# Kernel tuning notes

Hardware: AMD Instinct MI355X
Metric: run time of the kernel (lower is better)

Reference implementation:

```python
import jax, jax.numpy as jnp
import numpy as np

EPS = 1e-14  # clamp floor from torch .clamp(1e-14)


def setup_inputs() -> dict:
    key = jax.random.key(0)
    kq, kk, kv, km = jax.random.split(key, 4)
    B, L, D = 16, 2048, 64
    q = jax.random.normal(kq, (B, L, D), dtype=jnp.float32)
    k = jax.random.normal(kk, (B, L, D), dtype=jnp.float32)
    v = jax.random.normal(kv, (B, L, D), dtype=jnp.float32)
    # boolean mask, True = masked-out position (score forced to 0 in 'dot' mode)
    attn_mask = jax.random.randint(km, (B, L, L), 0, 2).astype(jnp.bool_)
    return {"q": q, "k": k, "v": v, "attn_mask": attn_mask}


def reference(q, k, v, attn_mask):
    # kernel_type='dot': raw QK^T scores (no temperature scaling)
    attn = jnp.einsum('bqd,bkd->bqk', q, k)
    # masked positions set to 0 (not -inf) in the 'dot' path
    attn = jnp.where(attn_mask, jnp.zeros((), attn.dtype), attn)
    # sum-normalization instead of softmax: attn / attn.sum(-1).clamp(1e-14)
    denom = jnp.clip(jnp.sum(attn, axis=2, keepdims=True), EPS)
    attn = attn / denom
    # dropout is identity at inference (eval mode)
    output = jnp.einsum('bqk,bkd->bqd', attn, v)
    return output, attn
```

## Files before the change

kernel.cpp:

```cpp
#include <hip/hip_runtime.h>

#define Bb 16
#define Lq 2048
#define Dd 64
#define QT 16
#define NT 512
#define NWIN 16
#define WINB 32768

typedef _Float16 f16x2 __attribute__((ext_vector_type(2)));
typedef _Float16 f16x8 __attribute__((ext_vector_type(8)));
typedef __attribute__((ext_vector_type(4))) float f32x4;
typedef __attribute__((ext_vector_type(2))) float f32x2;
typedef __attribute__((ext_vector_type(4))) unsigned int u32x4;
typedef __attribute__((ext_vector_type(2))) unsigned int u32x2;
typedef __attribute__((ext_vector_type(4))) int i32x4;
typedef unsigned long long u64;

union H8 { f16x8 v8; f16x2 h2[4]; unsigned int u[4]; u32x4 u4; };
union H1 { f16x2 h; unsigned int u; };

__device__ __forceinline__ f16x2 pkrtz(float a, float b) {
  return __builtin_bit_cast(f16x2, __builtin_amdgcn_cvt_pkrtz(a, b));
}
__device__ __forceinline__ f32x4 MF16(f16x8 a, f16x8 b, f32x4 c) {
  return __builtin_amdgcn_mfma_f32_16x16x32_f16(a, b, c, 0, 0, 0);
}
__device__ __forceinline__ f32x4 MFu(u32x4 a, const H8& b, f32x4 c) {
  return MF16(__builtin_bit_cast(f16x8, a), b.v8, c);
}
__device__ __forceinline__ void gl_lds16(const void* g, void* l) {
  __builtin_amdgcn_global_load_lds(
      (const __attribute__((address_space(1))) void*)g,
      (__attribute__((address_space(3))) void*)l, 16, 0, 0);
}

__global__ __launch_bounds__(256)
void sdpa_prep(const float* __restrict__ kg, const float* __restrict__ vg,
               u32x4* __restrict__ Kw4, u32x4* __restrict__ Vq)
{
  const int t = threadIdx.x, blk = blockIdx.x;
  if (blk < 1024) {
    const int row = blk * 32 + (t >> 3);
    const int oct = t & 7;
    const int b = row >> 11, r = row & 2047;
    const int win = r >> 7, rw = r & 127;
    const float* kp = kg + (size_t)row * Dd + oct * 8;
    f32x4 a = *(const f32x4*)kp;
    f32x4 c = *(const f32x4*)(kp + 4);
    H1 h0, h1, h2, h3, l0, l1, l2, l3;
    h0.h = pkrtz(a.x, a.y); l0.h = pkrtz(a.x - (float)h0.h.x, a.y - (float)h0.h.y);
    h1.h = pkrtz(a.z, a.w); l1.h = pkrtz(a.z - (float)h1.h.x, a.w - (float)h1.h.y);
    h2.h = pkrtz(c.x, c.y); l2.h = pkrtz(c.x - (float)h2.h.x, c.y - (float)h2.h.y);
    h3.h = pkrtz(c.z, c.w); l3.h = pkrtz(c.z - (float)h3.h.x, c.w - (float)h3.h.y);
    u32x4 hh = {h0.u, h1.u, h2.u, h3.u};
    u32x4 ll = {l0.u, l1.u, l2.u, l3.u};
    const int sl = oct ^ (rw & 7);
    const size_t base = ((size_t)((b * 16 + win) * 128 + rw)) * 16;
    Kw4[base + sl] = hh;
    Kw4[base + 8 + sl] = ll;
  } else {
    const int v_ = (blk - 1024) * 256 + t;
    const int ln = v_ & 15, nt = (v_ >> 4) & 3, u = (v_ >> 6) & 3;
    const int ks = (v_ >> 8) & 7, g = (v_ >> 11) & 7, b = v_ >> 14;
    const int r0 = g * 256 + ks * 16 + 4 * u;
    const float* vp = vg + ((size_t)b * Lq + r0) * Dd + nt * 16 + ln;
    H1 p0, p1, p2, p3;
    p0.h = pkrtz(vp[0],        vp[64]);
    p1.h = pkrtz(vp[128],      vp[192]);
    p2.h = pkrtz(vp[128 * 64], vp[129 * 64]);
    p3.h = pkrtz(vp[130 * 64], vp[131 * 64]);
    u32x4 o = {p0.u, p1.u, p2.u, p3.u};
    Vq[v_] = o;
  }
}

__global__ __launch_bounds__(NT, 4)
void sdpa_main(const float* __restrict__ qg, const char* __restrict__ Kw,
               const u32x4* __restrict__ Vqp, const i32x4* __restrict__ mg4,
               float* __restrict__ outO, float* __restrict__ outA)
{
  __shared__ alignas(16) char kbuf[2][WINB];
  __shared__ alignas(16) char qmbuf[4624];
  __shared__ float red[QT][8];
  __shared__ float dinv_s[QT];

  unsigned int (*Qh)[36] = (unsigned int (*)[36])qmbuf;
  unsigned int (*Ql)[36] = (unsigned int (*)[36])(qmbuf + 2304);
  u64 (*mbits)[34]       = (u64 (*)[34])qmbuf;

  const int tid = threadIdx.x;
  const int l   = tid & 63;
  const int ln  = l & 15;
  const int u   = l >> 4;
  const int w   = tid >> 6;
  const int bid = (int)(blockIdx.x % 8) * 256 + (int)(blockIdx.x / 8);
  const int b   = bid >> 7;
  const int q0  = (bid & 127) * QT;
  const int ks  = w;

  {
    int r = tid >> 5, d2 = tid & 31;
    f32x2 qv = *(const f32x2*)(qg + (size_t)(b * Lq + q0 + r) * Dd + 2 * d2);
    H1 h, lo;
    h.h  = pkrtz(qv.x, qv.y);
    lo.h = pkrtz(qv.x - (float)h.h.x, qv.y - (float)h.h.y);
    Qh[r][d2] = h.u;
    Ql[r][d2] = lo.u;
  }

  const char* kwb = Kw + (size_t)b * NWIN * WINB;
  auto STAGE = [&](int buf_, int win_) {
#pragma unroll
    for (int i = 0; i < 4; ++i)
      gl_lds16(kwb + (size_t)win_ * WINB + i * 8192 + w * 1024 + l * 16,
               &kbuf[buf_][i * 8192 + w * 1024]);
  };
  STAGE(0, 0);
  __syncthreads();

  H8 Bh0, Bh1, Bl0, Bl1;
  Bh0.u4 = *(const u32x4*)&Qh[ln][4 * u];
  Bh1.u4 = *(const u32x4*)&Qh[ln][16 + 4 * u];
  Bl0.u4 = *(const u32x4*)&Ql[ln][4 * u];
  Bl1.u4 = *(const u32x4*)&Ql[ln][16 + 4 * u];
  __syncthreads();

#pragma unroll
  for (int i = 0; i < 2; ++i) {
    const int row = 2 * w + i;
    const size_t rbase = (size_t)(b * Lq + q0 + row) * 512;
#pragma unroll
    for (int W = 0; W < 8; ++W) {
      i32x4 mm = __builtin_nontemporal_load(&mg4[rbase + W * 64 + l]);
      u64 b0 = __ballot(mm.x != 0);
      u64 b1 = __ballot(mm.y != 0);
      u64 b2 = __ballot(mm.z != 0);
      u64 b3 = __ballot(mm.w != 0);
      if (l < 4) mbits[row][W * 4 + l] = (l == 0) ? b0 : (l == 1) ? b1 : (l == 2) ? b2 : b3;
    }
  }
  __syncthreads();

  unsigned int su[NWIN][2];
  f32x4 pv[4] = {{0,0,0,0},{0,0,0,0},{0,0,0,0},{0,0,0,0}};
  float rs = 0.f;
  const int key = ln & 7;
  const int sh  = ks * 4 + u;
  u32x4 MA = {0,0,0,0}, MC = {0,0,0,0};
  u32x4 vbuf[4];

#pragma unroll
  for (int win = 0; win < NWIN; ++win) {
    const int cur = win & 1;
    if (win < NWIN - 1) STAGE(cur ^ 1, win + 1);

    if ((win & 1) == 0) {
      const int g = win >> 1;
      const u64* mr = &mbits[ln][g * 4];
      MA = *(const u32x4*)mr;
      MC = *(const u32x4*)(mr + 2);
      const u32x4* vq = Vqp + (size_t)b * 16384 + (((g * 8 + ks) * 4 + u) * 4) * 16 + ln;
#pragma unroll
      for (int nt = 0; nt < 4; ++nt) vbuf[nt] = vq[nt * 16];
    }
    unsigned mw0 = (win & 1) ? MA.y : MA.x;
    unsigned mw1 = (win & 1) ? MA.w : MA.z;
    unsigned mw2 = (win & 1) ? MC.y : MC.x;
    unsigned mw3 = (win & 1) ? MC.w : MC.z;

    {
      const int rw = ks * 16 + ln;
      const char* rp = &kbuf[cur][0] + rw * 256;
      u32x4 h0  = *(const u32x4*)(rp + ((u ^ key) << 4));
      u32x4 h1  = *(const u32x4*)(rp + (((4 + u) ^ key) << 4));
      u32x4 l0_ = *(const u32x4*)(rp + ((8 | (u ^ key)) << 4));
      u32x4 l1_ = *(const u32x4*)(rp + ((8 | ((4 + u) ^ key)) << 4));
      f32x4 acc = {0.f, 0.f, 0.f, 0.f};
      acc = MFu(h0, Bh0, acc);
      acc = MFu(h0, Bl0, acc);
      acc = MFu(l0_, Bh0, acc);
      acc = MFu(h1, Bh1, acc);
      acc = MFu(h1, Bl1, acc);
      acc = MFu(l1_, Bh1, acc);
      float s0 = ((mw0 >> sh) & 1u) ? 0.f : acc.x;
      float s1 = ((mw1 >> sh) & 1u) ? 0.f : acc.y;
      float s2 = ((mw2 >> sh) & 1u) ? 0.f : acc.z;
      float s3 = ((mw3 >> sh) & 1u) ? 0.f : acc.w;
      rs += (s0 + s1) + (s2 + s3);
      H1 p0, p1;
      p0.h = pkrtz(s0, s1); p1.h = pkrtz(s2, s3);
      su[win][0] = p0.u; su[win][1] = p1.u;
    }
    if (win & 1) {
      H8 aw;
      aw.u[0] = su[win - 1][0]; aw.u[1] = su[win - 1][1];
      aw.u[2] = su[win][0];     aw.u[3] = su[win][1];
      pv[0] = MF16(aw.v8, __builtin_bit_cast(f16x8, vbuf[0]), pv[0]);
      pv[1] = MF16(aw.v8, __builtin_bit_cast(f16x8, vbuf[1]), pv[1]);
      pv[2] = MF16(aw.v8, __builtin_bit_cast(f16x8, vbuf[2]), pv[2]);
      pv[3] = MF16(aw.v8, __builtin_bit_cast(f16x8, vbuf[3]), pv[3]);
    }
    __syncthreads();
  }

  rs += __shfl_xor(rs, 16);
  rs += __shfl_xor(rs, 32);
  if (l < 16) red[l][ks] = rs;
  {
    char* srow = &kbuf[0][0] + ln * 4096;
    const unsigned skey = (unsigned)ln << 3;
#pragma unroll
    for (int win = 0; win < NWIN; ++win) {
      unsigned Bo = 256u * win + 32u * ks + 8u * u;
      u32x2 pk2 = {su[win][0], su[win][1]};
      *(u32x2*)(srow + (Bo ^ skey)) = pk2;
    }
  }
  __syncthreads();
  if (tid < QT) {
    f32x4 r0 = *(const f32x4*)&red[tid][0];
    f32x4 r1 = *(const f32x4*)&red[tid][4];
    float s = ((r0.x + r0.y) + (r0.z + r0.w)) + ((r1.x + r1.y) + (r1.z + r1.w));
    dinv_s[tid] = 1.0f / fmaxf(s, 1e-14f);
  }
  __syncthreads();

  {
    const char* Sb = &kbuf[0][0];
#pragma unroll
    for (int r = 0; r < 2; ++r) {
      const int rr = 2 * w + r;
      const float dv = dinv_s[rr];
      const char* sr = Sb + rr * 4096;
      const unsigned rk = (unsigned)rr << 3;
      float* arow = outA + (size_t)(b * Lq + q0 + rr) * Lq;
#pragma unroll
      for (int m = 0; m < 8; ++m) {
        u32x2 pk = *(const u32x2*)(sr + ((unsigned)(512 * m + 8 * l) ^ rk));
        H1 a0, a1; a0.u = pk.x; a1.u = pk.y;
        f32x4 st = {(float)a0.h.x * dv, (float)a0.h.y * dv,
                    (float)a1.h.x * dv, (float)a1.h.y * dv};
        __builtin_nontemporal_store(st, (f32x4*)(arow + 256 * m + 4 * l));
      }
    }
  }
  __syncthreads();

  {
    float (*Or)[16][66] = (float (*)[16][66])&kbuf[0][0];
#pragma unroll
    for (int nt = 0; nt < 4; ++nt)
#pragma unroll
      for (int r2 = 0; r2 < 4; ++r2)
        Or[ks][4 * u + r2][16 * nt + ln] = pv[nt][r2];
    __syncthreads();
    {
      int q_ = tid >> 5, d = (tid & 31) * 2;
      float o0 = 0.f, o1 = 0.f;
#pragma unroll
      for (int k2 = 0; k2 < 8; ++k2) {
        o0 += Or[k2][q_][d];
        o1 += Or[k2][q_][d + 1];
      }
      float dvq = dinv_s[q_];
      f32x2 st = {o0 * dvq, o1 * dvq};
      *(f32x2*)(outO + (size_t)(b * Lq + q0 + q_) * Dd + d) = st;
    }
  }
}

extern "C" void kernel_launch(void* const* d_in, const int* in_sizes, int n_in,
                              void* d_out, int out_size, void* d_ws, size_t ws_size,
                              hipStream_t stream) {
  const float* q = (const float*)d_in[0];
  const float* k = (const float*)d_in[1];
  const float* v = (const float*)d_in[2];
  const int*   m = (const int*)d_in[3];
  float* outO = (float*)d_out;
  float* outA = outO + (size_t)Bb * Lq * Dd;

  char* ws = (char*)d_ws;
  u32x4* Kw4 = (u32x4*)ws;
  u32x4* Vq  = (u32x4*)(ws + (8u << 20));
  sdpa_prep<<<2048, 256, 0, stream>>>(k, v, Kw4, Vq);
  sdpa_main<<<Bb * (Lq / QT), NT, 0, stream>>>(q, (const char*)Kw4, Vq,
                                               (const i32x4*)m, outO, outA);
}
```

Measured before the change: 161.1 us.

## Single-buffer K windows to halve LDS and raise occupancy

Replaces the double-buffered 64KB K window staging with a single 33KB buffer. The next window is now loaded only after the current one is consumed, with an extra barrier. The launch-bounds occupancy hint goes from 4 to 8 blocks per CU. The attention-row writeout is split into two halves so the smaller buffer can hold the fp16 scores. The aim is more resident blocks to hide latency, at the cost of losing the in-block copy/compute overlap, adding barriers, and tighter register limits.

```diff
diff --git a/kernel.cpp b/kernel.cpp
--- a/kernel.cpp
+++ b/kernel.cpp
@@ -75,12 +75,12 @@
   }
 }
 
-__global__ __launch_bounds__(NT, 4)
+__global__ __launch_bounds__(NT, 8)
 void sdpa_main(const float* __restrict__ qg, const char* __restrict__ Kw,
                const u32x4* __restrict__ Vqp, const i32x4* __restrict__ mg4,
                float* __restrict__ outO, float* __restrict__ outA)
 {
-  __shared__ alignas(16) char kbuf[2][WINB];
+  __shared__ alignas(16) char kbuf[33792];
   __shared__ alignas(16) char qmbuf[4624];
   __shared__ float red[QT][8];
   __shared__ float dinv_s[QT];
@@ -110,13 +110,13 @@
   }
 
   const char* kwb = Kw + (size_t)b * NWIN * WINB;
-  auto STAGE = [&](int buf_, int win_) {
+  auto STAGE = [&](int win_) {
 #pragma unroll
     for (int i = 0; i < 4; ++i)
       gl_lds16(kwb + (size_t)win_ * WINB + i * 8192 + w * 1024 + l * 16,
-               &kbuf[buf_][i * 8192 + w * 1024]);
+               &kbuf[i * 8192 + w * 1024]);
   };
-  STAGE(0, 0);
+  STAGE(0);
   __syncthreads();
 
   H8 Bh0, Bh1, Bl0, Bl1;
@@ -152,9 +152,6 @@
 
 #pragma unroll
   for (int win = 0; win < NWIN; ++win) {
-    const int cur = win & 1;
-    if (win < NWIN - 1) STAGE(cur ^ 1, win + 1);
-
     if ((win & 1) == 0) {
       const int g = win >> 1;
       const u64* mr = &mbits[ln][g * 4];
@@ -171,7 +168,7 @@
 
     {
       const int rw = ks * 16 + ln;
-      const char* rp = &kbuf[cur][0] + rw * 256;
+      const char* rp = &kbuf[0] + rw * 256;
       u32x4 h0  = *(const u32x4*)(rp + ((u ^ key) << 4));
       u32x4 h1  = *(const u32x4*)(rp + (((4 + u) ^ key) << 4));
       u32x4 l0_ = *(const u32x4*)(rp + ((8 | (u ^ key)) << 4));
@@ -202,21 +199,15 @@
       pv[3] = MF16(aw.v8, __builtin_bit_cast(f16x8, vbuf[3]), pv[3]);
     }
     __syncthreads();
+    if (win < NWIN - 1) {
+      STAGE(win + 1);
+      __syncthreads();
+    }
   }
 
   rs += __shfl_xor(rs, 16);
   rs += __shfl_xor(rs, 32);
   if (l < 16) red[l][ks] = rs;
-  {
-    char* srow = &kbuf[0][0] + ln * 4096;
-    const unsigned skey = (unsigned)ln << 3;
-#pragma unroll
-    for (int win = 0; win < NWIN; ++win) {
-      unsigned Bo = 256u * win + 32u * ks + 8u * u;
-      u32x2 pk2 = {su[win][0], su[win][1]};
-      *(u32x2*)(srow + (Bo ^ skey)) = pk2;
-    }
-  }
   __syncthreads();
   if (tid < QT) {
     f32x4 r0 = *(const f32x4*)&red[tid][0];
@@ -226,13 +217,23 @@
   }
   __syncthreads();
 
-  {
-    const char* Sb = &kbuf[0][0];
-#pragma unroll
-    for (int r = 0; r < 2; ++r) {
-      const int rr = 2 * w + r;
+#pragma unroll
+  for (int half = 0; half < 2; ++half) {
+    if ((ln >> 3) == half) {
+      char* srow = &kbuf[0] + (ln & 7) * 4096;
+      const unsigned skey = (unsigned)ln << 3;
+#pragma unroll
+      for (int win = 0; win < NWIN; ++win) {
+        unsigned Bo = 256u * win + 32u * ks + 8u * u;
+        u32x2 pk2 = {su[win][0], su[win][1]};
+        *(u32x2*)(srow + (Bo ^ skey)) = pk2;
+      }
+    }
+    __syncthreads();
+    {
+      const int rr = 8 * half + w;
       const float dv = dinv_s[rr];
-      const char* sr = Sb + rr * 4096;
+      const char* sr = &kbuf[0] + w * 4096;
       const unsigned rk = (unsigned)rr << 3;
       float* arow = outA + (size_t)(b * Lq + q0 + rr) * Lq;
 #pragma unroll
@@ -244,11 +245,11 @@
         __builtin_nontemporal_store(st, (f32x4*)(arow + 256 * m + 4 * l));
       }
     }
-  }
-  __syncthreads();
+    __syncthreads();
+  }
 
   {
-    float (*Or)[16][66] = (float (*)[16][66])&kbuf[0][0];
+    float (*Or)[16][66] = (float (*)[16][66])&kbuf[0];
 #pragma unroll
     for (int nt = 0; nt < 4; ++nt)
 #pragma unroll
```

Result: slower. 534.0 us (+231.5%).
